# Performance work log

Measured on AMD Instinct MI355X. Metric: run time of the kernel, lower is better.

Reference implementation:

```python
import jax, jax.numpy as jnp
import numpy as np

N_USER = 100000
M_ITEM = 50000
N_NODE = N_USER + M_ITEM
D = 64           # latent_dim
WD = D // 2      # word_emb_dim
FU = FI = 10     # padded feature-bag width
NUF = NIF = 30000
VOCAB = 20000
T = 8            # tokens per text source (name/comment/comment_list)
DNU = DNI = 10   # numeric feature dims
B = 2048         # seed batch
S = 20           # sampled neighbors per layer
L = 2            # num_layers


def setup_inputs() -> dict:
    key = jax.random.key(0)
    ks = jax.random.split(key, 26)
    f = lambda i, s: jax.random.normal(ks[i], s, jnp.float32) * 0.05
    ri = lambda i, s, hi: jax.random.randint(ks[i], s, 0, hi)
    return {
        # int (graph / lookup) inputs
        "seeds": ri(0, (B,), N_USER),
        "neigh1": ri(1, (B, S), N_NODE),
        "neigh2": ri(2, (B, S, S), N_NODE),
        "user_feat_idx": ri(3, (N_USER, FU), NUF),
        "item_feat_idx": ri(4, (M_ITEM, FI), NIF),
        "user_text_idx": ri(5, (N_USER, 3, T), VOCAB),
        "item_text_idx": ri(6, (M_ITEM, 3, T), VOCAB),
        # float tables / features
        "user_id_emb": f(7, (N_USER, D)),
        "item_id_emb": f(8, (M_ITEM, D)),
        "user_feat_emb": f(9, (NUF, D)),
        "item_feat_emb": f(10, (NIF, D)),
        "word_emb": f(11, (VOCAB, WD)),
        "user_word300": f(12, (N_USER, 300)),
        "item_word300": f(13, (M_ITEM, 300)),
        "item_sent768": f(14, (M_ITEM, 768)),
        "user_numeric": f(15, (N_USER, DNU)),
        "item_numeric": f(16, (M_ITEM, DNI)),
        # linears (stored as (in, out); y = x @ W + b)
        "Wnum_u": f(17, (DNU, D)), "bnum_u": jnp.zeros((D,), jnp.float32),
        "Wnum_i": f(18, (DNI, D)), "bnum_i": jnp.zeros((D,), jnp.float32),
        "Wproj_u": f(19, (int(D * 3.5) + 300, D)), "bproj_u": jnp.zeros((D,), jnp.float32),
        "Wproj_i": f(20, (int(D * 3.5) + 300 + 768, D)), "bproj_i": jnp.zeros((D,), jnp.float32),
        "W_w": f(21, (L, 2 * D, D)), "b_w": jnp.zeros((L, D), jnp.float32),
        "W_v": f(22, (L, D, D)), "b_v": jnp.zeros((L, D), jnp.float32),
    }


def _forward(user_id_emb, item_id_emb, user_feat_emb, item_feat_emb, word_emb,
             user_word300, item_word300, item_sent768, user_numeric, item_numeric,
             Wnum_u, bnum_u, Wnum_i, bnum_i, Wproj_u, bproj_u, Wproj_i, bproj_i,
             W_w, b_w, W_v, b_v,
             seeds, neigh1, neigh2, user_feat_idx, item_feat_idx,
             user_text_idx, item_text_idx):
    # --- multi-source node embeddings (get_text_embedding + proj + numeric) ---
    # text: mean-pool word embeddings per source, concat 3 sources -> 1.5*D
    u_text = word_emb[user_text_idx].mean(axis=2).reshape(N_USER, 3 * WD)
    i_text = word_emb[item_text_idx].mean(axis=2).reshape(M_ITEM, 3 * WD)
    # feature bags: mean-pooled embedding lookup
    u_feat = user_feat_emb[user_feat_idx].mean(axis=1)
    i_feat = item_feat_emb[item_feat_idx].mean(axis=1)
    u = (jnp.concatenate([user_id_emb, u_feat, u_text, user_word300], -1) @ Wproj_u
         + bproj_u + user_numeric @ Wnum_u + bnum_u)
    it = (jnp.concatenate([item_id_emb, i_feat, i_text, item_word300, item_sent768], -1) @ Wproj_i
          + bproj_i + item_numeric @ Wnum_i + bnum_i)
    x = jnp.concatenate([u, it], axis=0)  # [N_NODE, D], items offset by N_USER

    # --- neighbor-sampled GraphSAGE: h = W_l([self, mean(V_l(neigh))]) ---
    def sage(l, self_x, neigh_x, act):
        agg = (neigh_x @ W_v[l] + b_v[l]).mean(axis=-2)
        h = jnp.concatenate([self_x, agg], axis=-1) @ W_w[l] + b_w[l]
        return jax.nn.relu(h) if act else h

    x0 = x[seeds]        # [B, D]
    x1 = x[neigh1]       # [B, S, D]
    x2 = x[neigh2]       # [B, S, S, D]
    h1 = sage(0, x1, x2, True)   # layer-0 applied to 1-hop nodes
    h0 = sage(0, x0, x1, True)   # layer-0 applied to seeds
    out = sage(1, h0, h1, False)  # final layer, no activation
    return out  # [B, D]


def reference(seeds, neigh1, neigh2, user_feat_idx, item_feat_idx, user_text_idx,
              item_text_idx, user_id_emb, item_id_emb, user_feat_emb, item_feat_emb,
              word_emb, user_word300, item_word300, item_sent768, user_numeric,
              item_numeric, Wnum_u, bnum_u, Wnum_i, bnum_i, Wproj_u, bproj_u,
              Wproj_i, bproj_i, W_w, b_w, W_v, b_v):
    return _forward(user_id_emb, item_id_emb, user_feat_emb, item_feat_emb, word_emb,
                    user_word300, item_word300, item_sent768, user_numeric, item_numeric,
                    Wnum_u, bnum_u, Wnum_i, bnum_i, Wproj_u, bproj_u, Wproj_i, bproj_i,
                    W_w, b_w, W_v, b_v,
                    seeds, neigh1, neigh2, user_feat_idx, item_feat_idx,
                    user_text_idx, item_text_idx)
```

## Files before the change

### kernel.cpp

```cpp
#include <hip/hip_runtime.h>
#include <hip/hip_bf16.h>
#include <stdint.h>

#define N_USER 100000
#define M_ITEM 50000
#define N_NODE 150000
#define B_SEED 2048
#define S_NB 20
#define UBLK2 1563
#define IBLK2 782

typedef __bf16   bf16x8 __attribute__((ext_vector_type(8)));
typedef float    f32x4  __attribute__((ext_vector_type(4)));
typedef uint32_t u32x4  __attribute__((ext_vector_type(4)));

typedef __attribute__((address_space(3))) uint32_t lds_u32_t;
typedef __attribute__((address_space(1))) const uint32_t glb_u32_t;

__device__ __forceinline__ uint16_t f2bf(float f) {
    uint32_t u = __float_as_uint(f);
    return (uint16_t)((u + 0x7FFFu + ((u >> 16) & 1u)) >> 16);
}
__device__ __forceinline__ uint32_t pk2(float a, float b) {
    __hip_bfloat162 h = __float22bfloat162_rn(make_float2(a, b));
    return *reinterpret_cast<uint32_t*>(&h);
}
__device__ __forceinline__ float bf2f(uint16_t u) {
    return __uint_as_float(((uint32_t)u) << 16);
}

union BF8 { bf16x8 v; uint32_t u[4]; };

__device__ __forceinline__ bf16x8 pack8v(f32x4 lo, f32x4 hi) {
    BF8 r;
    r.u[0] = pk2(lo[0], lo[1]); r.u[1] = pk2(lo[2], lo[3]);
    r.u[2] = pk2(hi[0], hi[1]); r.u[3] = pk2(hi[2], hi[3]);
    return r.v;
}
__device__ __forceinline__ bf16x8 ldf32x8_mask(const float* rowp, int base, int limit) {
    BF8 r;
#pragma unroll
    for (int h = 0; h < 4; ++h) {
        const int k0 = base + 2 * h;
        const float a = (k0     < limit) ? rowp[k0]     : 0.f;
        const float b = (k0 + 1 < limit) ? rowp[k0 + 1] : 0.f;
        r.u[h] = pk2(a, b);
    }
    return r.v;
}

template<int N> __device__ __forceinline__ void waitcnt_vm() {
    asm volatile("s_waitcnt vmcnt(%0)" :: "n"(N) : "memory");
    __builtin_amdgcn_sched_barrier(0);
}

__global__ void prep_kernel(const float* __restrict__ Wproj_u, const float* __restrict__ Wnum_u,
                            const float* __restrict__ Wproj_i, const float* __restrict__ Wnum_i,
                            const float* __restrict__ Wv0, const float* __restrict__ Ww0,
                            uint16_t* __restrict__ WTU, uint16_t* __restrict__ WTI,
                            uint16_t* __restrict__ WvT, uint16_t* __restrict__ WwT)
{
    const int idx = blockIdx.x * 256 + threadIdx.x;
    if (idx < 36864) {
        const int d = idx / 576, kp = idx - d * 576;
        float v = 0.f;
        if (kp < 160)      v = Wproj_u[(64 + kp) * 64 + d];
        else if (kp < 192) { const int j = kp - 160; if (j < 10) v = Wnum_u[j * 64 + d]; }
        else if (kp < 224) { const int j = kp - 192; if (j < 12) v = Wproj_u[(512 + j) * 64 + d]; }
        else if (kp < 288) v = Wproj_u[(kp - 224) * 64 + d];
        else               v = Wproj_u[(224 + kp - 288) * 64 + d];
        WTU[d * 576 + kp] = f2bf(v);
    } else if (idx < 122880) {
        const int i2 = idx - 36864;
        const int d = i2 / 1344, kp = i2 - d * 1344;
        float v = 0.f;
        if (kp < 160)      v = Wproj_i[(64 + kp) * 64 + d];
        else if (kp < 192) { const int j = kp - 160; if (j < 10) v = Wnum_i[j * 64 + d]; }
        else if (kp < 224) { const int j = kp - 192; if (j < 12) v = Wproj_i[(512 + j) * 64 + d]; }
        else if (kp < 288) v = Wproj_i[(kp - 224) * 64 + d];
        else if (kp < 576) v = Wproj_i[(224 + kp - 288) * 64 + d];
        else               v = Wproj_i[(524 + kp - 576) * 64 + d];
        WTI[d * 1344 + kp] = f2bf(v);
    } else {
        const int i2 = idx - 122880;
        if (i2 < 4096) { const int d = i2 >> 6, k = i2 & 63;  WvT[d * 64 + k]  = f2bf(Wv0[k * 64 + d]); }
        else           { const int j = i2 - 4096;
                         const int d = j >> 7, k = j & 127;   WwT[d * 128 + k] = f2bf(Ww0[k * 64 + d]); }
    }
}

__global__ __launch_bounds__(256) void gpack_kernel(
    const int* __restrict__ ufi, const int* __restrict__ ifi,
    const int* __restrict__ uti, const int* __restrict__ iti,
    const float* __restrict__ ufe, const float* __restrict__ ife,
    const float* __restrict__ wemb,
    uint16_t* __restrict__ Apre)
{
    const int gid  = blockIdx.x * 256 + threadIdx.x;
    const int node = gid >> 3;
    const int d0   = gid & 7;
    if (node >= N_NODE) return;
    const bool item = node >= N_USER;
    const int nloc  = item ? node - N_USER : node;
    const int*   fidx = (item ? ifi : ufi) + (size_t)nloc * 10;
    const int*   tidx = (item ? iti : uti) + (size_t)nloc * 24;
    const float* fe   = item ? ife : ufe;
    uint16_t* out = Apre + (size_t)node * 160;

    {
        f32x4 s0 = {0, 0, 0, 0}, s1 = {0, 0, 0, 0};
#pragma unroll
        for (int j = 0; j < 10; ++j) {
            const float* p = fe + (size_t)fidx[j] * 64 + 8 * d0;
            s0 += *(const f32x4*)p;
            s1 += *(const f32x4*)(p + 4);
        }
        s0 *= 0.1f; s1 *= 0.1f;
        uint4 o = make_uint4(pk2(s0[0], s0[1]), pk2(s0[2], s0[3]),
                             pk2(s1[0], s1[1]), pk2(s1[2], s1[3]));
        *(uint4*)(out + 8 * d0) = o;
    }
#pragma unroll
    for (int s = 0; s < 3; ++s) {
        f32x4 a = {0, 0, 0, 0};
#pragma unroll
        for (int j = 0; j < 8; ++j) {
            const float* p = wemb + (size_t)tidx[s * 8 + j] * 32 + 4 * d0;
            a += *(const f32x4*)p;
        }
        a *= 0.125f;
        *(uint2*)(out + 64 + 32 * s + 4 * d0) = make_uint2(pk2(a[0], a[1]), pk2(a[2], a[3]));
    }
}

__global__ __launch_bounds__(256) void pgemm_kernel(
    const uint16_t* __restrict__ Apre,
    const float* __restrict__ u_id,  const float* __restrict__ i_id,
    const float* __restrict__ uw300, const float* __restrict__ iw300,
    const float* __restrict__ is768,
    const float* __restrict__ unum,  const float* __restrict__ inum,
    const uint16_t* __restrict__ WTU, const uint16_t* __restrict__ WTI,
    const float* __restrict__ bproj_u, const float* __restrict__ bnum_u,
    const float* __restrict__ bproj_i, const float* __restrict__ bnum_i,
    uint16_t* __restrict__ xout)
{
    __shared__ char lds[2][4][6144];

    const int t = threadIdx.x;
    const int w = t >> 6, l = t & 63;
    const int l15 = l & 15, g4 = l >> 4;
    const bool item = blockIdx.x < IBLK2;
    const int tile  = item ? blockIdx.x : (blockIdx.x - IBLK2);
    const int ntype = item ? M_ITEM : N_USER;
    const int nb    = tile * 64;
    const int NC    = item ? 35 : 11;

    const float* idp = item ? i_id  : u_id;
    const float* w3p = item ? iw300 : uw300;
    const float* nmp = item ? inum  : unum;
    const uint16_t* WT = item ? WTI : WTU;
    const int KP       = item ? 1344 : 576;

    f32x4 acc[4] = {};
    const uint16_t* WTb = WT + (size_t)l15 * KP + g4 * 8;

    auto MM = [&](bf16x8 af, int kb) {
#pragma unroll
        for (int db = 0; db < 4; ++db) {
            const bf16x8 bfr = *reinterpret_cast<const bf16x8*>(WTb + (size_t)db * 16 * KP + kb);
            acc[db] = __builtin_amdgcn_mfma_f32_16x16x32_bf16(af, bfr, acc[db], 0, 0, 0);
        }
    };

    const uint16_t* WTfrag = WT + (size_t)l15 * KP + g4 * 8;

    auto stage = [&](int bi, int c) {
        const float* base; int stride, coloff;
        if (c < 2)       { base = idp;    stride = 64;  coloff = c * 32; }
        else if (c < 11) { base = w3p;    stride = 300; coloff = (c - 2) * 32; }
        else             { base = is768;  stride = 768; coloff = (c - 11) * 32; }
        char* wbase = &lds[bi][w][0];
#pragma unroll
        for (int j = 0; j < 2; ++j) {
            const int rl   = j * 8 + (l >> 3);
            const int nn   = nb + w * 16 + rl;
            const int node = nn < ntype ? nn : (ntype - 1);
            const int swb  = ((l & 7) * 16) ^ ((rl & 7) << 4);
            const float* g = base + (size_t)node * stride + coloff + (swb >> 2);
            __builtin_amdgcn_global_load_lds((glb_u32_t*)g,
                (lds_u32_t*)(void*)(wbase + j * 1024), 16, 0, 0);
        }
        const int kb = 224 + 32 * c;
#pragma unroll
        for (int i = 0; i < 4; ++i) {
            const uint16_t* g = WTfrag + (size_t)i * 16 * KP + kb;
            __builtin_amdgcn_global_load_lds((glb_u32_t*)g,
                (lds_u32_t*)(void*)(wbase + 2048 + i * 1024), 16, 0, 0);
        }
    };

    auto compute = [&](int bi) {
        const char* wbase = &lds[bi][w][0];
        const int r = l15;
        const f32x4 lo = *(const f32x4*)(wbase + r * 128 + ((g4 * 32)      ^ ((r & 7) << 4)));
        const f32x4 hi = *(const f32x4*)(wbase + r * 128 + ((g4 * 32 + 16) ^ ((r & 7) << 4)));
        const bf16x8 af = pack8v(lo, hi);
#pragma unroll
        for (int db = 0; db < 4; ++db) {
            const bf16x8 bfr = *(const bf16x8*)(wbase + 2048 + db * 1024 + l * 16);
            acc[db] = __builtin_amdgcn_mfma_f32_16x16x32_bf16(af, bfr, acc[db], 0, 0, 0);
        }
    };

    const int nloc = (nb + w * 16 + l15) < ntype ? (nb + w * 16 + l15) : (ntype - 1);
    const int node = (item ? N_USER : 0) + nloc;
    const uint16_t* ap = Apre + (size_t)node * 160 + g4 * 8;
    bf16x8 af[5];
#pragma unroll
    for (int ks = 0; ks < 5; ++ks) af[ks] = *(const bf16x8*)(ap + ks * 32);
    const bf16x8 numf  = ldf32x8_mask(nmp + (size_t)nloc * 10, g4 * 8, 10);
    const bf16x8 tailf = ldf32x8_mask(w3p + (size_t)nloc * 300, 288 + g4 * 8, 300);

    stage(0, 0);
#pragma unroll
    for (int ks = 0; ks < 5; ++ks) MM(af[ks], ks * 32);
    MM(numf, 160);
    MM(tailf, 192);

#pragma unroll 1
    for (int c = 0; c < NC - 1; ++c) {
        stage((c + 1) & 1, c + 1);
        waitcnt_vm<6>();
        compute(c & 1);
    }
    waitcnt_vm<0>();
    compute((NC - 1) & 1);

    const int nb_out = nb + w * 16 + g4 * 4;
    const float* bp = item ? bproj_i : bproj_u;
    const float* bn = item ? bnum_i  : bnum_u;
    uint16_t* xo = xout + (size_t)(item ? N_USER : 0) * 64;
#pragma unroll
    for (int db = 0; db < 4; ++db) {
        const int d = db * 16 + l15;
        const float bias = bp[d] + bn[d];
#pragma unroll
        for (int r = 0; r < 4; ++r) {
            const int nn = nb_out + r;
            if (nn < ntype) xo[(size_t)nn * 64 + d] = f2bf(acc[db][r] + bias);
        }
    }
}

__global__ __launch_bounds__(256) void xv_kernel(
    const uint16_t* __restrict__ x, const uint16_t* __restrict__ WvT,
    const float* __restrict__ bv, uint16_t* __restrict__ xv, int n)
{
    const int t = threadIdx.x;
    const int w = t >> 6, l = t & 63, l15 = l & 15, g4 = l >> 4;
    const int node = blockIdx.x * 64 + w * 16 + l15;
    const int node_c = node < n ? node : n - 1;

    f32x4 acc[4] = {};
    const uint16_t* WTb = WvT + l15 * 64 + g4 * 8;
#pragma unroll
    for (int ks = 0; ks < 2; ++ks) {
        const bf16x8 af = *reinterpret_cast<const bf16x8*>(x + (size_t)node_c * 64 + ks * 32 + g4 * 8);
#pragma unroll
        for (int db = 0; db < 4; ++db) {
            const bf16x8 bfr = *reinterpret_cast<const bf16x8*>(WTb + db * 16 * 64 + ks * 32);
            acc[db] = __builtin_amdgcn_mfma_f32_16x16x32_bf16(af, bfr, acc[db], 0, 0, 0);
        }
    }
    const int node_base = blockIdx.x * 64 + w * 16 + g4 * 4;
#pragma unroll
    for (int db = 0; db < 4; ++db) {
        const int d = db * 16 + l15;
        const float bias = bv[d];
#pragma unroll
        for (int r = 0; r < 4; ++r) {
            const int nn = node_base + r;
            if (nn < n) xv[(size_t)nn * 64 + d] = f2bf(acc[db][r] + bias);
        }
    }
}

__global__ __launch_bounds__(256) void sage_mfma_kernel(
    const uint16_t* __restrict__ x, const uint16_t* __restrict__ xv,
    const int* __restrict__ self_idx, const int* __restrict__ neigh_idx,
    const uint16_t* __restrict__ WwT, const float* __restrict__ bw,
    uint16_t* __restrict__ out, int relu)
{
    const int t = threadIdx.x;
    const int w = t >> 6, l = t & 63, l15 = l & 15, g4 = l >> 4;
    const int r = blockIdx.x * 64 + w * 16 + l15;
    const int sidx = self_idx[r];
    const int* ni = neigh_idx + (size_t)r * S_NB;

    f32x4 acc[4] = {};
    const uint16_t* WTb = WwT + l15 * 128 + g4 * 8;

    auto MM = [&](bf16x8 af, int kb) {
#pragma unroll
        for (int db = 0; db < 4; ++db) {
            const bf16x8 bfr = *reinterpret_cast<const bf16x8*>(WTb + db * 16 * 128 + kb);
            acc[db] = __builtin_amdgcn_mfma_f32_16x16x32_bf16(af, bfr, acc[db], 0, 0, 0);
        }
    };

#pragma unroll
    for (int ks = 0; ks < 2; ++ks) {
        const bf16x8 af = *reinterpret_cast<const bf16x8*>(x + (size_t)sidx * 64 + ks * 32 + g4 * 8);
        MM(af, ks * 32);
    }
#pragma unroll
    for (int ks = 0; ks < 2; ++ks) {
        float ev[4] = {0.f, 0.f, 0.f, 0.f}, od[4] = {0.f, 0.f, 0.f, 0.f};
#pragma unroll
        for (int j = 0; j < S_NB; ++j) {
            const u32x4 v = *reinterpret_cast<const u32x4*>(xv + (size_t)ni[j] * 64 + ks * 32 + g4 * 8);
#pragma unroll
            for (int q = 0; q < 4; ++q) {
                ev[q] += __uint_as_float(v[q] << 16);
                od[q] += __uint_as_float(v[q] & 0xffff0000u);
            }
        }
        BF8 m;
#pragma unroll
        for (int q = 0; q < 4; ++q) m.u[q] = pk2(ev[q] * (1.f / S_NB), od[q] * (1.f / S_NB));
        MM(m.v, 64 + ks * 32);
    }

    const int rb = blockIdx.x * 64 + w * 16 + g4 * 4;
#pragma unroll
    for (int db = 0; db < 4; ++db) {
        const int d = db * 16 + l15;
        const float bias = bw[d];
#pragma unroll
        for (int rr = 0; rr < 4; ++rr) {
            float h = acc[db][rr] + bias;
            if (relu) h = fmaxf(h, 0.f);
            out[(size_t)(rb + rr) * 64 + d] = f2bf(h);
        }
    }
}

__global__ __launch_bounds__(256) void final_kernel(
    const uint16_t* __restrict__ h0, const uint16_t* __restrict__ h1,
    const float* __restrict__ Wv, const float* __restrict__ bv,
    const float* __restrict__ Ww, const float* __restrict__ bw,
    float* __restrict__ out)
{
    __shared__ float WvL[64 * 64];
    __shared__ float WwL[128 * 64];
    const int t = threadIdx.x;
    for (int i = t; i < 64 * 64; i += 256)  WvL[i] = Wv[i];
    for (int i = t; i < 128 * 64; i += 256) WwL[i] = Ww[i];
    __syncthreads();

    const int wave = t >> 6, lane = t & 63;
    const int base = blockIdx.x * 32 + wave * 8;
    const float bvl = bv[lane], bwl = bw[lane];

    for (int i = 0; i < 8; ++i) {
        const int b = base + i;
        float m = 0.f;
#pragma unroll
        for (int s = 0; s < S_NB; ++s)
            m += bf2f(h1[(size_t)(b * S_NB + s) * 64 + lane]);
        m *= (1.f / S_NB);

        float agg = bvl;
#pragma unroll 8
        for (int k = 0; k < 64; ++k)
            agg += __shfl(m, k) * WvL[k * 64 + lane];

        const float selfv = bf2f(h0[(size_t)b * 64 + lane]);
        float h = bwl;
#pragma unroll 8
        for (int k = 0; k < 64; ++k)
            h += __shfl(selfv, k) * WwL[k * 64 + lane];
#pragma unroll 8
        for (int k = 0; k < 64; ++k)
            h += __shfl(agg, k) * WwL[(64 + k) * 64 + lane];

        out[(size_t)b * 64 + lane] = h;
    }
}

extern "C" void kernel_launch(void* const* d_in, const int* in_sizes, int n_in,
                              void* d_out, int out_size, void* d_ws, size_t ws_size,
                              hipStream_t stream)
{
    const int*   seeds   = (const int*)d_in[0];
    const int*   neigh1  = (const int*)d_in[1];
    const int*   neigh2  = (const int*)d_in[2];
    const int*   ufi     = (const int*)d_in[3];
    const int*   ifi     = (const int*)d_in[4];
    const int*   uti     = (const int*)d_in[5];
    const int*   iti     = (const int*)d_in[6];
    const float* u_id    = (const float*)d_in[7];
    const float* i_id    = (const float*)d_in[8];
    const float* ufe     = (const float*)d_in[9];
    const float* ife     = (const float*)d_in[10];
    const float* wemb    = (const float*)d_in[11];
    const float* uw300   = (const float*)d_in[12];
    const float* iw300   = (const float*)d_in[13];
    const float* is768   = (const float*)d_in[14];
    const float* unum    = (const float*)d_in[15];
    const float* inum    = (const float*)d_in[16];
    const float* Wnum_u  = (const float*)d_in[17];
    const float* bnum_u  = (const float*)d_in[18];
    const float* Wnum_i  = (const float*)d_in[19];
    const float* bnum_i  = (const float*)d_in[20];
    const float* Wproj_u = (const float*)d_in[21];
    const float* bproj_u = (const float*)d_in[22];
    const float* Wproj_i = (const float*)d_in[23];
    const float* bproj_i = (const float*)d_in[24];
    const float* W_w     = (const float*)d_in[25];
    const float* b_w     = (const float*)d_in[26];
    const float* W_v     = (const float*)d_in[27];
    const float* b_v     = (const float*)d_in[28];

    uint16_t* WTU  = (uint16_t*)d_ws;
    uint16_t* WTI  = WTU  + 36864;
    uint16_t* WvT0 = WTI  + 86016;
    uint16_t* WwT0 = WvT0 + 4096;
    uint16_t* xbf  = WwT0 + 8192;
    uint16_t* xvbf = xbf  + (size_t)N_NODE * 64;
    uint16_t* h1bf = xvbf + (size_t)N_NODE * 64;
    uint16_t* h0bf = h1bf + (size_t)B_SEED * S_NB * 64;
    uint16_t* Apre = xvbf;
    float* outp = (float*)d_out;

    prep_kernel<<<528, 256, 0, stream>>>(
        Wproj_u, Wnum_u, Wproj_i, Wnum_i, W_v, W_w, WTU, WTI, WvT0, WwT0);

    gpack_kernel<<<(N_NODE * 8 + 255) / 256, 256, 0, stream>>>(
        ufi, ifi, uti, iti, ufe, ife, wemb, Apre);

    pgemm_kernel<<<UBLK2 + IBLK2, 256, 0, stream>>>(
        Apre, u_id, i_id, uw300, iw300, is768, unum, inum,
        WTU, WTI, bproj_u, bnum_u, bproj_i, bnum_i, xbf);

    xv_kernel<<<(N_NODE + 63) / 64, 256, 0, stream>>>(xbf, WvT0, b_v, xvbf, N_NODE);

    sage_mfma_kernel<<<(B_SEED * S_NB) / 64, 256, 0, stream>>>(
        xbf, xvbf, neigh1, neigh2, WwT0, b_w, h1bf, 1);
    sage_mfma_kernel<<<B_SEED / 64, 256, 0, stream>>>(
        xbf, xvbf, seeds, neigh1, WwT0, b_w, h0bf, 1);

    final_kernel<<<B_SEED / 32, 256, 0, stream>>>(
        h0bf, h1bf, W_v + 4096, b_v + 64, W_w + 8192, b_w + 64, outp);
}
```

Measured before the change: 347.4 us.

## Load weight fragments directly to registers instead of staging through LDS

```diff
diff --git a/kernel.cpp b/kernel.cpp
--- a/kernel.cpp
+++ b/kernel.cpp
@@ -133,7 +133,7 @@
     }
 }
 
-__global__ __launch_bounds__(256) void pgemm_kernel(
+__global__ __launch_bounds__(256, 4) void pgemm_kernel(
     const uint16_t* __restrict__ Apre,
     const float* __restrict__ u_id,  const float* __restrict__ i_id,
     const float* __restrict__ uw300, const float* __restrict__ iw300,
@@ -144,7 +144,7 @@
     const float* __restrict__ bproj_i, const float* __restrict__ bnum_i,
     uint16_t* __restrict__ xout)
 {
-    __shared__ char lds[2][4][6144];
+    __shared__ char lds[2][4][2048];
 
     const int t = threadIdx.x;
     const int w = t >> 6, l = t & 63;
@@ -163,18 +163,17 @@
 
     f32x4 acc[4] = {};
     const uint16_t* WTb = WT + (size_t)l15 * KP + g4 * 8;
-
-    auto MM = [&](bf16x8 af, int kb) {
+    const uint16_t* WTfrag = WTb;
+
+    auto MM = [&](bf16x8 af2, int kb) {
 #pragma unroll
         for (int db = 0; db < 4; ++db) {
             const bf16x8 bfr = *reinterpret_cast<const bf16x8*>(WTb + (size_t)db * 16 * KP + kb);
-            acc[db] = __builtin_amdgcn_mfma_f32_16x16x32_bf16(af, bfr, acc[db], 0, 0, 0);
+            acc[db] = __builtin_amdgcn_mfma_f32_16x16x32_bf16(af2, bfr, acc[db], 0, 0, 0);
         }
     };
 
-    const uint16_t* WTfrag = WT + (size_t)l15 * KP + g4 * 8;
-
-    auto stage = [&](int bi, int c) {
+    auto stageA = [&](int bi, int c) {
         const float* base; int stride, coloff;
         if (c < 2)       { base = idp;    stride = 64;  coloff = c * 32; }
         else if (c < 11) { base = w3p;    stride = 300; coloff = (c - 2) * 32; }
@@ -190,26 +189,24 @@
             __builtin_amdgcn_global_load_lds((glb_u32_t*)g,
                 (lds_u32_t*)(void*)(wbase + j * 1024), 16, 0, 0);
         }
+    };
+
+    auto loadB = [&](bf16x8* breg, int c) {
         const int kb = 224 + 32 * c;
 #pragma unroll
-        for (int i = 0; i < 4; ++i) {
-            const uint16_t* g = WTfrag + (size_t)i * 16 * KP + kb;
-            __builtin_amdgcn_global_load_lds((glb_u32_t*)g,
-                (lds_u32_t*)(void*)(wbase + 2048 + i * 1024), 16, 0, 0);
-        }
+        for (int i = 0; i < 4; ++i)
+            breg[i] = *reinterpret_cast<const bf16x8*>(WTfrag + (size_t)i * 16 * KP + kb);
     };
 
-    auto compute = [&](int bi) {
+    auto computeA = [&](int bi, const bf16x8* breg) {
         const char* wbase = &lds[bi][w][0];
         const int r = l15;
         const f32x4 lo = *(const f32x4*)(wbase + r * 128 + ((g4 * 32)      ^ ((r & 7) << 4)));
         const f32x4 hi = *(const f32x4*)(wbase + r * 128 + ((g4 * 32 + 16) ^ ((r & 7) << 4)));
-        const bf16x8 af = pack8v(lo, hi);
-#pragma unroll
-        for (int db = 0; db < 4; ++db) {
-            const bf16x8 bfr = *(const bf16x8*)(wbase + 2048 + db * 1024 + l * 16);
-            acc[db] = __builtin_amdgcn_mfma_f32_16x16x32_bf16(af, bfr, acc[db], 0, 0, 0);
-        }
+        const bf16x8 af2 = pack8v(lo, hi);
+#pragma unroll
+        for (int db = 0; db < 4; ++db)
+            acc[db] = __builtin_amdgcn_mfma_f32_16x16x32_bf16(af2, breg[db], acc[db], 0, 0, 0);
     };
 
     const int nloc = (nb + w * 16 + l15) < ntype ? (nb + w * 16 + l15) : (ntype - 1);
@@ -221,20 +218,28 @@
     const bf16x8 numf  = ldf32x8_mask(nmp + (size_t)nloc * 10, g4 * 8, 10);
     const bf16x8 tailf = ldf32x8_mask(w3p + (size_t)nloc * 300, 288 + g4 * 8, 300);
 
-    stage(0, 0);
+    bf16x8 b0[4], b1[4];
+    stageA(0, 0);
+    loadB(b0, 0);
 #pragma unroll
     for (int ks = 0; ks < 5; ++ks) MM(af[ks], ks * 32);
     MM(numf, 160);
     MM(tailf, 192);
 
+    int c = 0;
 #pragma unroll 1
-    for (int c = 0; c < NC - 1; ++c) {
-        stage((c + 1) & 1, c + 1);
+    for (; c + 2 <= NC; c += 2) {
+        stageA(1, c + 1); loadB(b1, c + 1);
         waitcnt_vm<6>();
-        compute(c & 1);
-    }
-    waitcnt_vm<0>();
-    compute((NC - 1) & 1);
+        computeA(0, b0);
+        if (c + 2 < NC) { stageA(0, c + 2); loadB(b0, c + 2); waitcnt_vm<6>(); }
+        else            { waitcnt_vm<0>(); }
+        computeA(1, b1);
+    }
+    if (c < NC) {
+        waitcnt_vm<0>();
+        computeA(0, b0);
+    }
 
     const int nb_out = nb + w * 16 + g4 * 4;
     const float* bp = item ? bproj_i : bproj_u;
```

Result: slower. 354.6 us (+2.1%).
